# Kernel optimization log

Hardware: AMD Instinct MI355X
Metric: run time of the kernel (lower is better)

The kernel has to match this reference:

```python
import jax, jax.numpy as jnp
import numpy as np

D_MODEL = 1024
NUM_HEAD = 16
D_HEAD = 64
SEQ = 1024
MEM = 1024
BATCH = 4
LN_EPS = 1e-5


def _rel_shift(x):
    # x: [i, j, b, n] -- Transformer-XL relative shift trick
    i, j, b, n = x.shape
    zero_pad = jnp.zeros((i, 1, b, n), dtype=x.dtype)
    x_padded = jnp.concatenate([zero_pad, x], axis=1).reshape(j + 1, i, b, n)
    return x_padded[1:].reshape(i, j, b, n)


def setup_inputs() -> dict:
    key = jax.random.key(0)
    ks = jax.random.split(key, 8)
    w_scale = 1.0 / np.sqrt(D_MODEL)  # keep activations O(1)
    total = MEM + SEQ
    return {
        "x": jax.random.normal(ks[0], (SEQ, BATCH, D_MODEL), jnp.float32),
        "memory": jax.random.normal(ks[1], (MEM, BATCH, D_MODEL), jnp.float32),
        "pos_emb": jax.random.normal(ks[2], (total, BATCH, D_MODEL), jnp.float32),
        "pos_bias_u": jax.random.normal(ks[3], (NUM_HEAD, D_HEAD), jnp.float32) * 0.02,
        "pos_bias_v": jax.random.normal(ks[4], (NUM_HEAD, D_HEAD), jnp.float32) * 0.02,
        "W_qkv": jax.random.normal(ks[5], (3 * NUM_HEAD * D_HEAD, D_MODEL), jnp.float32) * w_scale,
        "W_rel": jax.random.normal(ks[6], (NUM_HEAD * D_HEAD, D_MODEL), jnp.float32) * w_scale,
        "W_o": jax.random.normal(ks[7], (D_MODEL, NUM_HEAD * D_HEAD), jnp.float32) * w_scale,
        "ln_gamma": jnp.ones((D_MODEL,), jnp.float32),
        "ln_beta": jnp.zeros((D_MODEL,), jnp.float32),
    }


def reference(x, memory, pos_emb, pos_bias_u, pos_bias_v, W_qkv, W_rel, W_o, ln_gamma, ln_beta):
    seq_len = x.shape[0]
    c = jnp.concatenate([memory, x], axis=0)        # [T, B, D]
    T, B = c.shape[0], c.shape[1]
    n, d = pos_bias_u.shape
    scale = 1.0 / np.sqrt(d)

    heads = c @ W_qkv.T                              # [T, B, 3*n*d]
    q, k, v = jnp.split(heads, 3, axis=-1)
    q = q.reshape(T, B, n, d)[-seq_len:]             # [S, B, n, d]
    k = k.reshape(T, B, n, d)                        # [T, B, n, d]
    v = v.reshape(T, B, n, d)
    r = (pos_emb @ W_rel.T).reshape(T, B, n, d)      # [T, B, n, d]

    AC = jnp.einsum('ibnd,jbnd->ijbn', q + pos_bias_u, k)
    BD = _rel_shift(jnp.einsum('ibnd,jbnd->ijbn', q + pos_bias_v, r))
    attn_score = (AC + BD) * scale                   # [S, T, B, n]
    attn_prob = jax.nn.softmax(attn_score, axis=1)   # softmax over key dim (dropout = eval identity)

    attn_vec = jnp.einsum('ijbn,jbnd->ibnd', attn_prob, v).reshape(seq_len, B, n * d)
    attn_out = attn_vec @ W_o.T                      # [S, B, D]

    y = x + attn_out
    mu = jnp.mean(y, axis=-1, keepdims=True)
    var = jnp.mean(jnp.square(y - mu), axis=-1, keepdims=True)
    return ln_gamma * (y - mu) / jnp.sqrt(var + LN_EPS) + ln_beta
```

## Files before the change

kernel.cpp:

```cpp
#include <hip/hip_runtime.h>

#define S_ 1024
#define M_ 1024
#define T_ 2048
#define B_ 4
#define H_ 16
#define DM_ 1024
#define DH_ 64

typedef __attribute__((ext_vector_type(8))) short s16x8;
typedef __attribute__((ext_vector_type(16))) float f32x16;

__device__ __forceinline__ unsigned short f2b(float x){
  unsigned int u = __float_as_uint(x);
  u = (u + 0x7fffu + ((u>>16)&1u)) >> 16;
  return (unsigned short)u;
}
__device__ __forceinline__ float b2f(unsigned short h){
  return __uint_as_float(((unsigned int)h)<<16);
}
__device__ __forceinline__ uint4 pack8(const float* v){
  uint4 o;
  o.x = (unsigned)f2b(v[0]) | ((unsigned)f2b(v[1])<<16);
  o.y = (unsigned)f2b(v[2]) | ((unsigned)f2b(v[3])<<16);
  o.z = (unsigned)f2b(v[4]) | ((unsigned)f2b(v[5])<<16);
  o.w = (unsigned)f2b(v[6]) | ((unsigned)f2b(v[7])<<16);
  return o;
}
__device__ __forceinline__ void glds16(const unsigned short* g, unsigned short* l){
  __builtin_amdgcn_global_load_lds((const __attribute__((address_space(1))) void*)g,
                                   (__attribute__((address_space(3))) void*)l, 16, 0, 0);
}

#define BAR_L()   asm volatile("s_waitcnt lgkmcnt(0)\ns_barrier" ::: "memory")
#define BAR_VL()  asm volatile("s_waitcnt vmcnt(0) lgkmcnt(0)\ns_barrier" ::: "memory")
#define BAR_V6L() asm volatile("s_waitcnt vmcnt(6) lgkmcnt(0)\ns_barrier" ::: "memory")

__global__ __launch_bounds__(256) void cast_all(
    const float* __restrict__ mem, const float* __restrict__ x,
    const float* __restrict__ pos, const float* __restrict__ wqkv,
    const float* __restrict__ wrel, const float* __restrict__ wo,
    unsigned short* __restrict__ c16, unsigned short* __restrict__ pos16,
    unsigned short* __restrict__ wq16, unsigned short* __restrict__ wr16,
    unsigned short* __restrict__ wo16)
{
  int u = blockIdx.x*256 + threadIdx.x;
  const float* s; unsigned short* d;
  if (u < 1048576)      { s = (u < 524288) ? mem + (size_t)u*8 : x + (size_t)(u-524288)*8;
                          d = c16 + (size_t)u*8; }
  else if (u < 2097152) { int v = u - 1048576; s = pos  + (size_t)v*8; d = pos16 + (size_t)v*8; }
  else if (u < 2490368) { int v = u - 2097152; s = wqkv + (size_t)v*8; d = wq16  + (size_t)v*8; }
  else if (u < 2621440) { int v = u - 2490368; s = wrel + (size_t)v*8; d = wr16  + (size_t)v*8; }
  else                  { int v = u - 2621440; s = wo   + (size_t)v*8; d = wo16  + (size_t)v*8; }
  float4 x0 = *(const float4*)s;
  float4 x1 = *(const float4*)(s+4);
  float f[8] = {x0.x,x0.y,x0.z,x0.w,x1.x,x1.y,x1.z,x1.w};
  *(uint4*)d = pack8(f);
}

__global__ __launch_bounds__(256) void gemm_nt(const unsigned short* __restrict__ A,
    const unsigned short* __restrict__ Bw, void* __restrict__ Cout,
    const float* __restrict__ res, int Ntot, int K, int mode)
{
  __shared__ __align__(16) unsigned short a_s[128*64];
  __shared__ __align__(16) unsigned short b_s[128*64];
  const int tid = threadIdx.x;
  const int lane = tid & 63, wave = tid >> 6;
  const int wr = wave >> 1, wc = wave & 1;
  const long m0 = (long)blockIdx.y * 128, n0 = (long)blockIdx.x * 128;
  f32x16 acc[2][2];
  for (int qa=0;qa<2;qa++) for(int qb=0;qb<2;qb++) for (int e=0;e<16;e++) acc[qa][qb][e]=0.f;
  int srow[4], scol[4];
  for (int c = 0; c < 4; c++) {
    int ch = c*256 + tid;
    srow[c] = ch >> 3;
    scol[c] = (((ch & 7) ^ (srow[c] & 7))) * 8;
  }
  for (int k0 = 0; k0 < K; k0 += 64) {
    for (int c = 0; c < 4; c++) {
      int ch = c*256 + tid;
      glds16(&A[(size_t)(m0+srow[c])*K + k0 + scol[c]], &a_s[ch*8]);
      glds16(&Bw[(size_t)(n0+srow[c])*K + k0 + scol[c]], &b_s[ch*8]);
    }
    __syncthreads();
    for (int ks = 0; ks < 4; ks++) {
      const int kb = ks*2 + (lane>>5);
      s16x8 af[2], bf[2];
      for (int q = 0; q < 2; q++) {
        int ra = wr*64 + q*32 + (lane&31);
        int rb = wc*64 + q*32 + (lane&31);
        af[q] = *(const s16x8*)&a_s[ra*64 + ((kb ^ (ra&7))<<3)];
        bf[q] = *(const s16x8*)&b_s[rb*64 + ((kb ^ (rb&7))<<3)];
      }
      for (int qr=0;qr<2;qr++)
        for (int qc2=0;qc2<2;qc2++)
          acc[qr][qc2] = __builtin_amdgcn_mfma_f32_32x32x16_bf16(af[qr], bf[qc2], acc[qr][qc2], 0,0,0);
    }
    __syncthreads();
  }
  for (int qr=0;qr<2;qr++)
    for (int qc2=0;qc2<2;qc2++)
      for (int e=0;e<16;e++){
        long row = m0 + wr*64 + qr*32 + (e&3) + 8*(e>>2) + 4*(lane>>5);
        long col = n0 + wc*64 + qc2*32 + (lane&31);
        size_t o = (size_t)row*Ntot + col;
        if (mode == 0) ((unsigned short*)Cout)[o] = f2b(acc[qr][qc2][e]);
        else           ((float*)Cout)[o] = acc[qr][qc2][e] + res[o];
      }
}

__global__ __launch_bounds__(256) void scatter_quv(const unsigned short* __restrict__ qkvo,
   const float* __restrict__ u, const float* __restrict__ v,
   unsigned short* __restrict__ QU, unsigned short* __restrict__ QV)
{
  int gid = blockIdx.x*256 + threadIdx.x;
  int d0 = (gid & 7) * 8;
  int i  = (gid >> 3) & (S_-1);
  int bh = gid >> 13;
  int b = bh >> 4, h = bh & 15;
  size_t src = (size_t)((M_+i)*B_ + b)*3072 + h*64 + d0;
  uint4 q8 = *(const uint4*)&qkvo[src];
  float f[8];
  f[0]=b2f(q8.x&0xffff); f[1]=b2f(q8.x>>16); f[2]=b2f(q8.y&0xffff); f[3]=b2f(q8.y>>16);
  f[4]=b2f(q8.z&0xffff); f[5]=b2f(q8.z>>16); f[6]=b2f(q8.w&0xffff); f[7]=b2f(q8.w>>16);
  float fu[8], fv[8];
  for (int e=0;e<8;e++){ fu[e] = f[e] + u[h*64+d0+e]; fv[e] = f[e] + v[h*64+d0+e]; }
  size_t dst = ((size_t)bh*S_ + i)*64 + d0;
  *(uint4*)&QU[dst] = pack8(fu);
  *(uint4*)&QV[dst] = pack8(fv);
}

__global__ __launch_bounds__(256) void scatter_vt(const unsigned short* __restrict__ qkvo,
    unsigned short* __restrict__ VT)
{
  __shared__ __align__(16) unsigned short v_s[64*72];
  const int tid = threadIdx.x;
  const int bh = blockIdx.x, b = bh>>4, h = bh&15;
  const int t0 = blockIdx.y*64;
  const unsigned short* Vg = qkvo + (size_t)b*3072 + 2048 + h*64;
  for (int c=0;c<2;c++){
    int ch = c*256 + tid;
    int r = ch>>3, off = (ch&7)*8;
    *(uint4*)&v_s[r*72+off] = *(const uint4*)&Vg[(size_t)(t0+r)*12288 + off];
  }
  __syncthreads();
  for (int c=0;c<2;c++){
    int ch = c*256 + tid;
    int d = ch>>3, toff = (ch&7)*8;
    unsigned short vals[8];
    for (int e=0;e<8;e++) vals[e] = v_s[(toff+e)*72 + d];
    uint4 pk;
    pk.x = (unsigned)vals[0] | ((unsigned)vals[1]<<16);
    pk.y = (unsigned)vals[2] | ((unsigned)vals[3]<<16);
    pk.z = (unsigned)vals[4] | ((unsigned)vals[5]<<16);
    pk.w = (unsigned)vals[6] | ((unsigned)vals[7]<<16);
    *(uint4*)&VT[((size_t)bh*64 + d)*T_ + t0 + toff] = pk;
  }
}

__global__ __launch_bounds__(256,2) void flash_attn4(
    const unsigned short* __restrict__ QU, const unsigned short* __restrict__ QV,
    const unsigned short* __restrict__ qkvo, const unsigned short* __restrict__ VT,
    const unsigned short* __restrict__ relo, unsigned short* __restrict__ AV)
{
  __shared__ __align__(16) unsigned short qv_s[65*72];
  __shared__ __align__(16) unsigned short k_s [2][64*64];
  __shared__ __align__(16) unsigned short vt_s[64*64];
  __shared__ __align__(16) unsigned short rg_s[2][128*64];
  __shared__ __align__(16) unsigned short p_s [64*64];
  __shared__ float l_s[64];

  const int tid = threadIdx.x, lane = tid&63, wave = tid>>6;
  const int bh = blockIdx.x, b = bh>>4, h = bh&15;
  const int i0 = blockIdx.y*64;
  const int qr = wave>>1, qc = wave&1;
  const int hi = lane>>5, ll = lane&31;
  const unsigned short* QUb = QU + (size_t)bh*S_*DH_;
  const unsigned short* QVb = QV + (size_t)bh*S_*DH_;
  const unsigned short* Kg  = qkvo + (size_t)b*3072 + 1024 + h*64;
  const unsigned short* VTb = VT + (size_t)bh*64*T_;
  const unsigned short* Rg  = relo + (size_t)b*1024 + h*64;

  const int s0r = tid>>3,        s0c = (((tid&7)       ^ (s0r&7)))*8;
  const int s1r = (256+tid)>>3,  s1c = ((((256+tid)&7) ^ (s1r&7)))*8;

  glds16(&Kg [(size_t)(0+s0r)*12288 + s0c], &k_s[0][(size_t)tid*8]);
  glds16(&Kg [(size_t)(0+s1r)*12288 + s1c], &k_s[0][(size_t)(256+tid)*8]);
  {
    const int wb0 = 0 - i0 + 960;
    for (int c=0;c<4;c++){
      int ch = c*256+tid; int rr = ch>>3, off = ch&7;
      int t = wb0 + rr; t = t < 0 ? 0 : (t > T_-1 ? T_-1 : t);
      glds16(&Rg[(size_t)t*4096 + ((off ^ (rr&7)))*8], &rg_s[0][(size_t)ch*8]);
    }
  }
  for (int c=0;c<2;c++){
    int ch = c*256+tid; int row = ch>>3, off=(ch&7);
    *(uint4*)&p_s[row*64 + ((off ^ (row&7))<<3)] = *(const uint4*)&QUb[(size_t)(i0+row)*64 + off*8];
    *(uint4*)&qv_s[row*72+off*8] = *(const uint4*)&QVb[(size_t)(i0+row)*64 + off*8];
  }
  if (tid < 8) {
    int rr = i0 + 64; if (rr > S_-1) rr = S_-1;
    *(uint4*)&qv_s[64*72 + tid*8] = *(const uint4*)&QVb[(size_t)rr*64 + tid*8];
  }
  BAR_L();

  s16x8 qur0, qur1, qur2, qur3;
  s16x8 qv00, qv01, qv02, qv03;
  {
    const int rq = qr*32 + ll;
    qur0 = *(const s16x8*)&p_s[rq*64 + (((0*2+hi) ^ (rq&7))<<3)];
    qur1 = *(const s16x8*)&p_s[rq*64 + (((1*2+hi) ^ (rq&7))<<3)];
    qur2 = *(const s16x8*)&p_s[rq*64 + (((2*2+hi) ^ (rq&7))<<3)];
    qur3 = *(const s16x8*)&p_s[rq*64 + (((3*2+hi) ^ (rq&7))<<3)];
    const int ro = rq*72 + hi*8;
    qv00 = *(const s16x8*)&qv_s[ro +  0];
    qv01 = *(const s16x8*)&qv_s[ro + 16];
    qv02 = *(const s16x8*)&qv_s[ro + 32];
    qv03 = *(const s16x8*)&qv_s[ro + 48];
  }

  s16x8 ones;
  for (int e=0;e<8;e++) ones[e] = (short)0x3F80;

  f32x16 acc_o, acc_l;
  for (int e=0;e<16;e++){ acc_o[e]=0.f; acc_l[e]=0.f; }

  const int col = qc*32 + ll;
  const int cbase = (qc - qr + 1) * 32;

  int cur = 0;
  for (int j0 = 0; j0 < T_; j0 += 64) {
    const int jdmax = j0 + 63 - i0;
    const int jdmin = j0 - 63 - i0;
    const int cls = (jdmax <= 1024) ? 0 : ((jdmin >= 1026) ? 2 : 1);
    const int jn = j0 + 64;
    unsigned short* kc = &k_s[cur][0];
    unsigned short* rc = &rg_s[cur][0];
    unsigned short* kn = &k_s[cur^1][0];
    unsigned short* rn = &rg_s[cur^1][0];

    BAR_VL();

    glds16(&VTb[(size_t)s0r*T_ + j0 + s0c], &vt_s[(size_t)tid*8]);
    glds16(&VTb[(size_t)s1r*T_ + j0 + s1c], &vt_s[(size_t)(256+tid)*8]);
    if (jn < T_) {
      glds16(&Kg[(size_t)(jn+s0r)*12288 + s0c], &kn[(size_t)tid*8]);
      glds16(&Kg[(size_t)(jn+s1r)*12288 + s1c], &kn[(size_t)(256+tid)*8]);
      const int jdmaxn = jn + 63 - i0;
      const int jdminn = jn - 63 - i0;
      const int clsn = (jdmaxn <= 1024) ? 0 : ((jdminn >= 1026) ? 2 : 1);
      const int wbn = (clsn == 2) ? (jn - i0 - 1089) : (jn - i0 + 960);
      for (int c=0;c<4;c++){
        int ch = c*256+tid; int rr = ch>>3, off = ch&7;
        int t = wbn + rr; t = t < 0 ? 0 : (t > T_-1 ? T_-1 : t);
        glds16(&Rg[(size_t)t*4096 + ((off ^ (rr&7)))*8], &rn[(size_t)ch*8]);
      }
    }

    s16x8 av0, av1, av2, av3;
    if (cls == 2) {
      const int ro1 = (qr*32+ll+1)*72 + hi*8;
      av0 = *(const s16x8*)&qv_s[ro1 +  0];
      av1 = *(const s16x8*)&qv_s[ro1 + 16];
      av2 = *(const s16x8*)&qv_s[ro1 + 32];
      av3 = *(const s16x8*)&qv_s[ro1 + 48];
    } else {
      av0 = qv00; av1 = qv01; av2 = qv02; av3 = qv03;
    }

    f32x16 gacc0, gacc1;
    for (int e=0;e<16;e++){ gacc0[e]=0.f; gacc1[e]=0.f; }
    __builtin_amdgcn_s_setprio(1);
#define BANDK(KS, AV) { \
      int kb = KS*2 + hi; \
      { int br = cbase + ll; \
        s16x8 bb = *(const s16x8*)&rc[br*64 + ((kb ^ (br&7))<<3)]; \
        gacc0 = __builtin_amdgcn_mfma_f32_32x32x16_bf16(AV, bb, gacc0, 0,0,0); } \
      { int br = cbase + 32 + ll; \
        s16x8 bb = *(const s16x8*)&rc[br*64 + ((kb ^ (br&7))<<3)]; \
        gacc1 = __builtin_amdgcn_mfma_f32_32x32x16_bf16(AV, bb, gacc1, 0,0,0); } }
    BANDK(0, av0) BANDK(1, av1) BANDK(2, av2) BANDK(3, av3)

    f32x16 acc;
    for (int e=0;e<16;e++) acc[e]=0.f;
#define ACK(KS, AU) { \
      int kb = KS*2 + hi; \
      int rbk = qc*32 + ll; \
      s16x8 bq = *(const s16x8*)&kc[rbk*64 + ((kb ^ (rbk&7))<<3)]; \
      acc = __builtin_amdgcn_mfma_f32_32x32x16_bf16(AU, bq, acc, 0,0,0); }
    ACK(0, qur0) ACK(1, qur1) ACK(2, qur2) ACK(3, qur3)
    __builtin_amdgcn_s_setprio(0);

    for (int e=0;e<16;e++){
      int rm = 4*hi + (e&3) + 8*(e>>2);
      int r  = qr*32 + rm;
      int jd = j0 + col - (i0 + r);
      int tl = (ll + rm + 1) & 31;
      float sel = (tl > rm) ? gacc1[e] : gacc0[e];
      int li = ((((ll - rm + 31) & 31) | (hi<<5)) << 2);
      float bd = __uint_as_float((unsigned)__builtin_amdgcn_ds_bpermute(li, (int)__float_as_uint(sel)));
      if (jd == 1025) bd = 0.f;
      float p = __expf((acc[e] + bd) * 0.125f);
      if (!(cls == 1 && jd >= 1026))
        p_s[r*64 + (((col>>3) ^ (r&7))<<3) + (col&7)] = f2b(p);
    }

    if (cls == 1) {
      BAR_L();
      const int wb2 = j0 - i0 - 1089;
      for (int c=0;c<4;c++){
        int ch = c*256+tid; int rr = ch>>3, off = ch&7;
        int t = wb2 + rr; t = t < 0 ? 0 : (t > T_-1 ? T_-1 : t);
        glds16(&Rg[(size_t)t*4096 + ((off ^ (rr&7)))*8], &rc[(size_t)ch*8]);
      }
      BAR_VL();
      f32x16 g2a, g2b;
      for (int e=0;e<16;e++){ g2a[e]=0.f; g2b[e]=0.f; }
      __builtin_amdgcn_s_setprio(1);
#define BANDW(KS) { \
        int kb = KS*2 + hi; \
        const int ro1 = (qr*32+ll+1)*72 + hi*8; \
        s16x8 a = *(const s16x8*)&qv_s[ro1 + KS*16]; \
        { int br = cbase + ll; \
          s16x8 bb = *(const s16x8*)&rc[br*64 + ((kb ^ (br&7))<<3)]; \
          g2a = __builtin_amdgcn_mfma_f32_32x32x16_bf16(a, bb, g2a, 0,0,0); } \
        { int br = cbase + 32 + ll; \
          s16x8 bb = *(const s16x8*)&rc[br*64 + ((kb ^ (br&7))<<3)]; \
          g2b = __builtin_amdgcn_mfma_f32_32x32x16_bf16(a, bb, g2b, 0,0,0); } }
      BANDW(0) BANDW(1) BANDW(2) BANDW(3)
      __builtin_amdgcn_s_setprio(0);
      for (int e=0;e<16;e++){
        int rm = 4*hi + (e&3) + 8*(e>>2);
        int r  = qr*32 + rm;
        int jd = j0 + col - (i0 + r);
        int tl = (ll + rm + 1) & 31;
        float sel = (tl > rm) ? g2b[e] : g2a[e];
        int li = ((((ll - rm + 31) & 31) | (hi<<5)) << 2);
        float bd = __uint_as_float((unsigned)__builtin_amdgcn_ds_bpermute(li, (int)__float_as_uint(sel)));
        float p = __expf((acc[e] + bd) * 0.125f);
        if (jd >= 1026)
          p_s[r*64 + (((col>>3) ^ (r&7))<<3) + (col&7)] = f2b(p);
      }
    }

    if (jn < T_) { BAR_V6L(); } else { BAR_VL(); }

    __builtin_amdgcn_s_setprio(1);
    for (int ks=0; ks<4; ks++){
      int kb = ks*2 + hi;
      int rv = qr*32 + ll, rbv = qc*32 + ll;
      s16x8 a  = *(const s16x8*)&p_s[rv*64 + ((kb ^ (rv&7))<<3)];
      s16x8 bv = *(const s16x8*)&vt_s[rbv*64 + ((kb ^ (rbv&7))<<3)];
      acc_o = __builtin_amdgcn_mfma_f32_32x32x16_bf16(a, bv, acc_o, 0,0,0);
      acc_l = __builtin_amdgcn_mfma_f32_32x32x16_bf16(a, ones, acc_l, 0,0,0);
    }
    __builtin_amdgcn_s_setprio(0);
    cur ^= 1;
  }

  if (qc == 0 && ll == 0) {
    for (int e=0;e<16;e++){
      int r = qr*32 + 4*hi + (e&3) + 8*(e>>2);
      l_s[r] = acc_l[e];
    }
  }
  BAR_L();
  for (int e=0;e<16;e++){
    int r = qr*32 + 4*hi + (e&3) + 8*(e>>2);
    float oo = acc_o[e] / l_s[r];
    AV[ ((size_t)(i0+r)*B_ + b)*(H_*DH_) + h*DH_ + col ] = f2b(oo);
  }
#undef BANDK
#undef ACK
#undef BANDW
}

__global__ __launch_bounds__(256) void ln_kernel(const float* __restrict__ y,
    const float* __restrict__ g, const float* __restrict__ be, float* __restrict__ o)
{
  __shared__ float red[8];
  int row = blockIdx.x, tid = threadIdx.x;
  const float* yr = y + (size_t)row*DM_;
  float v[4];
  for (int e=0;e<4;e++) v[e] = yr[tid + 256*e];
  float s = v[0]+v[1]+v[2]+v[3];
  for (int off=32; off>0; off>>=1) s += __shfl_down(s, off, 64);
  if ((tid&63)==0) red[tid>>6] = s;
  __syncthreads();
  if (tid==0) red[4] = red[0]+red[1]+red[2]+red[3];
  __syncthreads();
  float mu = red[4] * (1.f/DM_);
  __syncthreads();
  float q = 0.f;
  for (int e=0;e<4;e++){ float d = v[e]-mu; q += d*d; }
  for (int off=32; off>0; off>>=1) q += __shfl_down(q, off, 64);
  if ((tid&63)==0) red[tid>>6] = q;
  __syncthreads();
  if (tid==0) red[4] = red[0]+red[1]+red[2]+red[3];
  __syncthreads();
  float rstd = rsqrtf(red[4]*(1.f/DM_) + 1e-5f);
  for (int e=0;e<4;e++){
    int c = tid + 256*e;
    o[(size_t)row*DM_ + c] = g[c]*(v[e]-mu)*rstd + be[c];
  }
}

extern "C" void kernel_launch(void* const* d_in, const int* in_sizes, int n_in,
                              void* d_out, int out_size, void* d_ws, size_t ws_size,
                              hipStream_t stream)
{
  const float* x    = (const float*)d_in[0];
  const float* mem  = (const float*)d_in[1];
  const float* pos  = (const float*)d_in[2];
  const float* pbu  = (const float*)d_in[3];
  const float* pbv  = (const float*)d_in[4];
  const float* wqkv = (const float*)d_in[5];
  const float* wrel = (const float*)d_in[6];
  const float* wo   = (const float*)d_in[7];
  const float* gam  = (const float*)d_in[8];
  const float* bet  = (const float*)d_in[9];
  float* out = (float*)d_out;

  char* w = (char*)d_ws;
  unsigned short* qkvo  = (unsigned short*)(w + 0);
  unsigned short* relo  = (unsigned short*)(w + 50331648);
  unsigned short* wo16  = (unsigned short*)(w + 67108864);
  unsigned short* QUb   = (unsigned short*)(w + 69206016);
  unsigned short* QVb   = (unsigned short*)(w + 77594624);
  unsigned short* VT    = (unsigned short*)(w + 85983232);
  unsigned short* av16  = (unsigned short*)(w + 102760448);
  float*          yf    = (float*)(w + 111149056);
  unsigned short* c16   = (unsigned short*)(w + 127926272);
  unsigned short* pos16 = (unsigned short*)(w + 144703488);
  unsigned short* wq16  = (unsigned short*)(w + 161480704);
  unsigned short* wr16  = (unsigned short*)(w + 167772160);

  cast_all<<<10752, 256, 0, stream>>>(mem, x, pos, wqkv, wrel, wo,
                                      c16, pos16, wq16, wr16, wo16);

  gemm_nt<<<dim3(24,64), 256, 0, stream>>>(c16,   wq16, (void*)qkvo, nullptr, 3072, 1024, 0);
  gemm_nt<<<dim3(8,64),  256, 0, stream>>>(pos16, wr16, (void*)relo, nullptr, 1024, 1024, 0);

  scatter_quv<<<2048, 256, 0, stream>>>(qkvo, pbu, pbv, QUb, QVb);
  scatter_vt<<<dim3(64,32), 256, 0, stream>>>(qkvo, VT);

  flash_attn4<<<dim3(64,16), 256, 0, stream>>>(QUb, QVb, qkvo, VT, relo, av16);

  gemm_nt<<<dim3(8,32), 256, 0, stream>>>(av16, wo16, (void*)yf, x, 1024, 1024, 1);
  ln_kernel<<<4096, 256, 0, stream>>>(yf, gam, bet, out);
}
```

Before: 470.9 us.

## Split QKV projection into K, transposed-V, and Q GEMMs with fused epilogues

Replaces the single fused QKV GEMM and the two scatter kernels with three separate GEMMs. K is written compactly, V is produced directly in transposed per-head layout by swapping operands, and Q is computed only for the current segment with the pos_bias_u/v adds fused into the epilogue. This skips the unused Q projection over memory rows and removes the intermediate write and re-read of the full qkv buffer. The cost is that gemm_vt and gemm_q do strided, uncoalesced 2-byte scattered stores, and the work is spread over more launches.

```diff
diff --git a/kernel.cpp b/kernel.cpp
--- a/kernel.cpp
+++ b/kernel.cpp
@@ -109,58 +109,111 @@
       }
 }
 
-__global__ __launch_bounds__(256) void scatter_quv(const unsigned short* __restrict__ qkvo,
-   const float* __restrict__ u, const float* __restrict__ v,
-   unsigned short* __restrict__ QU, unsigned short* __restrict__ QV)
-{
-  int gid = blockIdx.x*256 + threadIdx.x;
-  int d0 = (gid & 7) * 8;
-  int i  = (gid >> 3) & (S_-1);
-  int bh = gid >> 13;
-  int b = bh >> 4, h = bh & 15;
-  size_t src = (size_t)((M_+i)*B_ + b)*3072 + h*64 + d0;
-  uint4 q8 = *(const uint4*)&qkvo[src];
-  float f[8];
-  f[0]=b2f(q8.x&0xffff); f[1]=b2f(q8.x>>16); f[2]=b2f(q8.y&0xffff); f[3]=b2f(q8.y>>16);
-  f[4]=b2f(q8.z&0xffff); f[5]=b2f(q8.z>>16); f[6]=b2f(q8.w&0xffff); f[7]=b2f(q8.w>>16);
-  float fu[8], fv[8];
-  for (int e=0;e<8;e++){ fu[e] = f[e] + u[h*64+d0+e]; fv[e] = f[e] + v[h*64+d0+e]; }
-  size_t dst = ((size_t)bh*S_ + i)*64 + d0;
-  *(uint4*)&QU[dst] = pack8(fu);
-  *(uint4*)&QV[dst] = pack8(fv);
-}
-
-__global__ __launch_bounds__(256) void scatter_vt(const unsigned short* __restrict__ qkvo,
-    unsigned short* __restrict__ VT)
-{
-  __shared__ __align__(16) unsigned short v_s[64*72];
+__global__ __launch_bounds__(256) void gemm_vt(const unsigned short* __restrict__ A,
+    const unsigned short* __restrict__ Bw, unsigned short* __restrict__ VT)
+{
+  __shared__ __align__(16) unsigned short a_s[128*64];
+  __shared__ __align__(16) unsigned short b_s[128*64];
   const int tid = threadIdx.x;
-  const int bh = blockIdx.x, b = bh>>4, h = bh&15;
-  const int t0 = blockIdx.y*64;
-  const unsigned short* Vg = qkvo + (size_t)b*3072 + 2048 + h*64;
-  for (int c=0;c<2;c++){
+  const int lane = tid & 63, wave = tid >> 6;
+  const int wr = wave >> 1, wc = wave & 1;
+  const int bz = blockIdx.z;
+  const long m0 = (long)blockIdx.y * 128, n0 = (long)blockIdx.x * 128;
+  f32x16 acc[2][2];
+  for (int qa=0;qa<2;qa++) for(int qb=0;qb<2;qb++) for (int e=0;e<16;e++) acc[qa][qb][e]=0.f;
+  int srow[4], scol[4];
+  for (int c = 0; c < 4; c++) {
     int ch = c*256 + tid;
-    int r = ch>>3, off = (ch&7)*8;
-    *(uint4*)&v_s[r*72+off] = *(const uint4*)&Vg[(size_t)(t0+r)*12288 + off];
-  }
-  __syncthreads();
-  for (int c=0;c<2;c++){
+    srow[c] = ch >> 3;
+    scol[c] = (((ch & 7) ^ (srow[c] & 7))) * 8;
+  }
+  for (int k0 = 0; k0 < 1024; k0 += 64) {
+    for (int c = 0; c < 4; c++) {
+      int ch = c*256 + tid;
+      glds16(&A[(size_t)(m0+srow[c])*1024 + k0 + scol[c]], &a_s[ch*8]);
+      glds16(&Bw[((size_t)(n0+srow[c])*4 + bz)*1024 + k0 + scol[c]], &b_s[ch*8]);
+    }
+    __syncthreads();
+    for (int ks = 0; ks < 4; ks++) {
+      const int kb = ks*2 + (lane>>5);
+      s16x8 af[2], bf[2];
+      for (int q = 0; q < 2; q++) {
+        int ra = wr*64 + q*32 + (lane&31);
+        int rb = wc*64 + q*32 + (lane&31);
+        af[q] = *(const s16x8*)&a_s[ra*64 + ((kb ^ (ra&7))<<3)];
+        bf[q] = *(const s16x8*)&b_s[rb*64 + ((kb ^ (rb&7))<<3)];
+      }
+      for (int qr=0;qr<2;qr++)
+        for (int qc2=0;qc2<2;qc2++)
+          acc[qr][qc2] = __builtin_amdgcn_mfma_f32_32x32x16_bf16(af[qr], bf[qc2], acc[qr][qc2], 0,0,0);
+    }
+    __syncthreads();
+  }
+  for (int qr=0;qr<2;qr++)
+    for (int qc2=0;qc2<2;qc2++)
+      for (int e=0;e<16;e++){
+        long row = m0 + wr*64 + qr*32 + (e&3) + 8*(e>>2) + 4*(lane>>5);
+        long col = n0 + wc*64 + qc2*32 + (lane&31);
+        VT[(size_t)bz*2097152 + (size_t)row*2048 + col] = f2b(acc[qr][qc2][e]);
+      }
+}
+
+__global__ __launch_bounds__(256) void gemm_q(const unsigned short* __restrict__ A,
+    const unsigned short* __restrict__ Bw, const float* __restrict__ u,
+    const float* __restrict__ v, unsigned short* __restrict__ QU,
+    unsigned short* __restrict__ QV)
+{
+  __shared__ __align__(16) unsigned short a_s[128*64];
+  __shared__ __align__(16) unsigned short b_s[128*64];
+  const int tid = threadIdx.x;
+  const int lane = tid & 63, wave = tid >> 6;
+  const int wr = wave >> 1, wc = wave & 1;
+  const long m0 = (long)blockIdx.y * 128, n0 = (long)blockIdx.x * 128;
+  f32x16 acc[2][2];
+  for (int qa=0;qa<2;qa++) for(int qb=0;qb<2;qb++) for (int e=0;e<16;e++) acc[qa][qb][e]=0.f;
+  int srow[4], scol[4];
+  for (int c = 0; c < 4; c++) {
     int ch = c*256 + tid;
-    int d = ch>>3, toff = (ch&7)*8;
-    unsigned short vals[8];
-    for (int e=0;e<8;e++) vals[e] = v_s[(toff+e)*72 + d];
-    uint4 pk;
-    pk.x = (unsigned)vals[0] | ((unsigned)vals[1]<<16);
-    pk.y = (unsigned)vals[2] | ((unsigned)vals[3]<<16);
-    pk.z = (unsigned)vals[4] | ((unsigned)vals[5]<<16);
-    pk.w = (unsigned)vals[6] | ((unsigned)vals[7]<<16);
-    *(uint4*)&VT[((size_t)bh*64 + d)*T_ + t0 + toff] = pk;
-  }
+    srow[c] = ch >> 3;
+    scol[c] = (((ch & 7) ^ (srow[c] & 7))) * 8;
+  }
+  for (int k0 = 0; k0 < 1024; k0 += 64) {
+    for (int c = 0; c < 4; c++) {
+      int ch = c*256 + tid;
+      glds16(&A[(size_t)(m0+srow[c])*1024 + k0 + scol[c]], &a_s[ch*8]);
+      glds16(&Bw[(size_t)(n0+srow[c])*1024 + k0 + scol[c]], &b_s[ch*8]);
+    }
+    __syncthreads();
+    for (int ks = 0; ks < 4; ks++) {
+      const int kb = ks*2 + (lane>>5);
+      s16x8 af[2], bf[2];
+      for (int q = 0; q < 2; q++) {
+        int ra = wr*64 + q*32 + (lane&31);
+        int rb = wc*64 + q*32 + (lane&31);
+        af[q] = *(const s16x8*)&a_s[ra*64 + ((kb ^ (ra&7))<<3)];
+        bf[q] = *(const s16x8*)&b_s[rb*64 + ((kb ^ (rb&7))<<3)];
+      }
+      for (int qr=0;qr<2;qr++)
+        for (int qc2=0;qc2<2;qc2++)
+          acc[qr][qc2] = __builtin_amdgcn_mfma_f32_32x32x16_bf16(af[qr], bf[qc2], acc[qr][qc2], 0,0,0);
+    }
+    __syncthreads();
+  }
+  for (int qr=0;qr<2;qr++)
+    for (int qc2=0;qc2<2;qc2++)
+      for (int e=0;e<16;e++){
+        long row = m0 + wr*64 + qr*32 + (e&3) + 8*(e>>2) + 4*(lane>>5);
+        long col = n0 + wc*64 + qc2*32 + (lane&31);
+        size_t dst = (((size_t)(row&3)*16 + (col>>6))*1024 + (row>>2))*64 + (col&63);
+        float a = acc[qr][qc2][e];
+        QU[dst] = f2b(a + u[col]);
+        QV[dst] = f2b(a + v[col]);
+      }
 }
 
 __global__ __launch_bounds__(256,2) void flash_attn4(
     const unsigned short* __restrict__ QU, const unsigned short* __restrict__ QV,
-    const unsigned short* __restrict__ qkvo, const unsigned short* __restrict__ VT,
+    const unsigned short* __restrict__ Kb, const unsigned short* __restrict__ VT,
     const unsigned short* __restrict__ relo, unsigned short* __restrict__ AV)
 {
   __shared__ __align__(16) unsigned short qv_s[65*72];
@@ -177,15 +230,15 @@
   const int hi = lane>>5, ll = lane&31;
   const unsigned short* QUb = QU + (size_t)bh*S_*DH_;
   const unsigned short* QVb = QV + (size_t)bh*S_*DH_;
-  const unsigned short* Kg  = qkvo + (size_t)b*3072 + 1024 + h*64;
+  const unsigned short* Kg  = Kb + (size_t)b*1024 + h*64;
   const unsigned short* VTb = VT + (size_t)bh*64*T_;
   const unsigned short* Rg  = relo + (size_t)b*1024 + h*64;
 
   const int s0r = tid>>3,        s0c = (((tid&7)       ^ (s0r&7)))*8;
   const int s1r = (256+tid)>>3,  s1c = ((((256+tid)&7) ^ (s1r&7)))*8;
 
-  glds16(&Kg [(size_t)(0+s0r)*12288 + s0c], &k_s[0][(size_t)tid*8]);
-  glds16(&Kg [(size_t)(0+s1r)*12288 + s1c], &k_s[0][(size_t)(256+tid)*8]);
+  glds16(&Kg [(size_t)(0+s0r)*4096 + s0c], &k_s[0][(size_t)tid*8]);
+  glds16(&Kg [(size_t)(0+s1r)*4096 + s1c], &k_s[0][(size_t)(256+tid)*8]);
   {
     const int wb0 = 0 - i0 + 960;
     for (int c=0;c<4;c++){
@@ -245,8 +298,8 @@
     glds16(&VTb[(size_t)s0r*T_ + j0 + s0c], &vt_s[(size_t)tid*8]);
     glds16(&VTb[(size_t)s1r*T_ + j0 + s1c], &vt_s[(size_t)(256+tid)*8]);
     if (jn < T_) {
-      glds16(&Kg[(size_t)(jn+s0r)*12288 + s0c], &kn[(size_t)tid*8]);
-      glds16(&Kg[(size_t)(jn+s1r)*12288 + s1c], &kn[(size_t)(256+tid)*8]);
+      glds16(&Kg[(size_t)(jn+s0r)*4096 + s0c], &kn[(size_t)tid*8]);
+      glds16(&Kg[(size_t)(jn+s1r)*4096 + s1c], &kn[(size_t)(256+tid)*8]);
       const int jdmaxn = jn + 63 - i0;
       const int jdminn = jn - 63 - i0;
       const int clsn = (jdmaxn <= 1024) ? 0 : ((jdminn >= 1026) ? 2 : 1);
@@ -423,29 +476,30 @@
   float* out = (float*)d_out;
 
   char* w = (char*)d_ws;
-  unsigned short* qkvo  = (unsigned short*)(w + 0);
-  unsigned short* relo  = (unsigned short*)(w + 50331648);
-  unsigned short* wo16  = (unsigned short*)(w + 67108864);
-  unsigned short* QUb   = (unsigned short*)(w + 69206016);
-  unsigned short* QVb   = (unsigned short*)(w + 77594624);
-  unsigned short* VT    = (unsigned short*)(w + 85983232);
-  unsigned short* av16  = (unsigned short*)(w + 102760448);
-  float*          yf    = (float*)(w + 111149056);
-  unsigned short* c16   = (unsigned short*)(w + 127926272);
-  unsigned short* pos16 = (unsigned short*)(w + 144703488);
-  unsigned short* wq16  = (unsigned short*)(w + 161480704);
-  unsigned short* wr16  = (unsigned short*)(w + 167772160);
+  unsigned short* Kb    = (unsigned short*)(w + 0);
+  unsigned short* relo  = (unsigned short*)(w + 16777216);
+  unsigned short* wo16  = (unsigned short*)(w + 33554432);
+  unsigned short* QUb   = (unsigned short*)(w + 35651584);
+  unsigned short* QVb   = (unsigned short*)(w + 44040192);
+  unsigned short* VT    = (unsigned short*)(w + 52428800);
+  unsigned short* av16  = (unsigned short*)(w + 69206016);
+  float*          yf    = (float*)(w + 77594624);
+  unsigned short* c16   = (unsigned short*)(w + 94371840);
+  unsigned short* pos16 = (unsigned short*)(w + 111149056);
+  unsigned short* wq16  = (unsigned short*)(w + 127926272);
+  unsigned short* wr16  = (unsigned short*)(w + 134217728);
 
   cast_all<<<10752, 256, 0, stream>>>(mem, x, pos, wqkv, wrel, wo,
                                       c16, pos16, wq16, wr16, wo16);
 
-  gemm_nt<<<dim3(24,64), 256, 0, stream>>>(c16,   wq16, (void*)qkvo, nullptr, 3072, 1024, 0);
-  gemm_nt<<<dim3(8,64),  256, 0, stream>>>(pos16, wr16, (void*)relo, nullptr, 1024, 1024, 0);
-
-  scatter_quv<<<2048, 256, 0, stream>>>(qkvo, pbu, pbv, QUb, QVb);
-  scatter_vt<<<dim3(64,32), 256, 0, stream>>>(qkvo, VT);
-
-  flash_attn4<<<dim3(64,16), 256, 0, stream>>>(QUb, QVb, qkvo, VT, relo, av16);
+  gemm_nt<<<dim3(8,64), 256, 0, stream>>>(c16, wq16 + (size_t)1024*1024,
+                                          (void*)Kb, nullptr, 1024, 1024, 0);
+  gemm_vt<<<dim3(16,8,4), 256, 0, stream>>>(wq16 + (size_t)2048*1024, c16, VT);
+  gemm_q<<<dim3(8,32), 256, 0, stream>>>(c16 + (size_t)4096*1024, wq16,
+                                         pbu, pbv, QUb, QVb);
+  gemm_nt<<<dim3(8,64), 256, 0, stream>>>(pos16, wr16, (void*)relo, nullptr, 1024, 1024, 0);
+
+  flash_attn4<<<dim3(64,16), 256, 0, stream>>>(QUb, QVb, Kb, VT, relo, av16);
 
   gemm_nt<<<dim3(8,32), 256, 0, stream>>>(av16, wo16, (void*)yf, x, 1024, 1024, 1);
   ln_kernel<<<4096, 256, 0, stream>>>(yf, gam, bet, out);
```

Result: faster. 455.5 us (-3.3%).
